# Kernel optimization log

Hardware: AMD Instinct MI355X
Metric: run time of the kernel (lower is better)

The kernel has to match this reference:

```python
import jax, jax.numpy as jnp
import numpy as np

LMAX = 5
L = LMAX + 1            # L_out = L_in = 6
DIM = L * L             # 36 spherical-harmonic coefficients
RES_B = 2 * L           # 12 beta points (Gauss-Legendre in cos(beta))
RES_A = 2 * L           # 12 alpha points (uniform)
CORRELATION = 3
REPEATS = np.arange(1, 2 * L, 2)  # [1,3,5,7,9,11]: ir.dim per l, mul=1 in irreps_out


def _normalized_assoc_legendre(lmax, x):
    """Fully (L2 on sphere) normalized associated Legendre Pbar_l^m(x), no CS phase.
    Returns dict[(l,m)] -> np.ndarray over x."""
    P = {}
    s = np.sqrt(np.maximum(1.0 - x * x, 0.0))
    P[(0, 0)] = np.full_like(x, np.sqrt(1.0 / (4.0 * np.pi)))
    for m in range(1, lmax + 1):
        P[(m, m)] = np.sqrt((2.0 * m + 1.0) / (2.0 * m)) * s * P[(m - 1, m - 1)]
    for m in range(0, lmax):
        P[(m + 1, m)] = np.sqrt(2.0 * m + 3.0) * x * P[(m, m)]
    for m in range(0, lmax + 1):
        for l in range(m + 2, lmax + 1):
            a = np.sqrt((4.0 * l * l - 1.0) / (l * l - m * m))
            b = np.sqrt(((l - 1.0) ** 2 - m * m) / (4.0 * (l - 1.0) ** 2 - 1.0))
            P[(l, m)] = a * (x * P[(l - 1, m)] - b * P[(l - 2, m)])
    return P


def build_s2grid(lmax, res_beta, res_alpha):
    """Y: [res_beta, res_alpha, (lmax+1)^2] real orthonormal SH samples.
    Yw: Y with quadrature weights so that einsum(f, Yw) inverts einsum(c, Y)."""
    xq, wq = np.polynomial.legendre.leggauss(res_beta)  # nodes in cos(beta)
    alpha = np.arange(res_alpha) * (2.0 * np.pi / res_alpha)
    P = _normalized_assoc_legendre(lmax, xq)
    dim = (lmax + 1) ** 2
    Y = np.zeros((res_beta, res_alpha, dim))
    sqrt2 = np.sqrt(2.0)
    for l in range(lmax + 1):
        for m in range(-l, l + 1):
            idx = l * l + l + m
            plm = P[(l, abs(m))]
            if m > 0:
                ang = sqrt2 * np.cos(m * alpha)
            elif m == 0:
                ang = np.ones(res_alpha)
            else:
                ang = sqrt2 * np.sin(-m * alpha)
            Y[:, :, idx] = plm[:, None] * ang[None, :]
    Yw = Y * wq[:, None, None] * (2.0 * np.pi / res_alpha)
    return jnp.asarray(Y, jnp.float32), jnp.asarray(Yw, jnp.float32)


def setup_inputs() -> dict:
    key = jax.random.key(0)
    k1, k2, k3 = jax.random.split(key, 3)
    atom_feat = jax.random.normal(k1, (4096, 128, DIM), dtype=jnp.float32)
    atom_type = jax.random.uniform(k2, (4096, 10), dtype=jnp.float32)
    weights = jax.random.normal(k3, (CORRELATION, 10, 128, L), dtype=jnp.float32)
    return {"atom_feat": atom_feat, "atom_type": atom_type, "weights": weights}


def reference(atom_feat, atom_type, weights):
    Y, Yw = build_s2grid(LMAX, RES_B, RES_A)

    def to_grid(c):      # [n, C, DIM] -> [n, C, beta, alpha]
        return jnp.einsum('nck,bak->ncba', c, Y)

    def from_grid(f):    # [n, C, beta, alpha] -> [n, C, DIM]
        return jnp.einsum('ncba,bak->nck', f, Yw)

    def apply_w(w):      # w: [E, C, L]; atom-type-weighted, expanded to DIM
        wn = jnp.einsum('ne,ecl->ncl', atom_type, w)  # [n, C, L]
        return jnp.repeat(wn, REPEATS, axis=-1, total_repeat_length=DIM)

    feat_grid = to_grid(atom_feat)  # reused across correlation orders
    prod = atom_feat
    result = apply_w(weights[0]) * prod
    for nu in range(1, CORRELATION):
        # Gaunt tensor product via S2 grid: pointwise multiply on the sphere
        prod = from_grid(to_grid(prod) * feat_grid)
        result = result + apply_w(weights[nu]) * prod
    return jnp.squeeze(result)
```

## Files before the change

### kernel.cpp

```cpp
#include <hip/hip_runtime.h>
#include <stdint.h>

namespace ct {

constexpr double PI_ = 3.14159265358979323846;

constexpr double csqrt(double x) {
  double g = x > 1.0 ? x : 1.0;
  for (int i = 0; i < 40; ++i) g = 0.5 * (g + x / g);
  return g;
}
constexpr double ccos(double x) {
  double x2 = x * x, t = 1.0, s = 1.0;
  for (int k = 1; k <= 16; ++k) { t *= -x2 / ((2.0 * k - 1.0) * (2.0 * k)); s += t; }
  return s;
}
constexpr double csin(double x) {
  double x2 = x * x, t = x, s = x;
  for (int k = 1; k <= 16; ++k) { t *= -x2 / ((2.0 * k) * (2.0 * k + 1.0)); s += t; }
  return s;
}

struct GL { double x[12]; double w[12]; };

constexpr GL gl12() {
  GL g{};
  for (int i = 0; i < 12; ++i) {
    double x = ccos(PI_ * (i + 0.75) / 12.5);
    for (int it = 0; it < 50; ++it) {
      double p0 = 1.0, p1 = x;
      for (int k = 2; k <= 12; ++k) { double pk = ((2.0 * k - 1.0) * x * p1 - (k - 1.0) * p0) / k; p0 = p1; p1 = pk; }
      double dp = 12.0 * (x * p1 - p0) / (x * x - 1.0);
      x -= p1 / dp;
    }
    double p0 = 1.0, p1 = x;
    for (int k = 2; k <= 12; ++k) { double pk = ((2.0 * k - 1.0) * x * p1 - (k - 1.0) * p0) / k; p0 = p1; p1 = pk; }
    double dp = 12.0 * (x * p1 - p0) / (x * x - 1.0);
    g.x[i] = x;
    g.w[i] = 2.0 / ((1.0 - x * x) * dp * dp);
  }
  return g;
}

struct Tab {
  double PA[12][36];
  double PB[12][36];
  double ANG[12][36];
};

constexpr Tab make_tab() {
  Tab t{};
  GL g = gl12();
  for (int b = 0; b < 12; ++b) {
    double x = g.x[b];
    double s = csqrt(1.0 - x * x);
    double P[6][6] = {};
    P[0][0] = csqrt(1.0 / (4.0 * PI_));
    for (int m = 1; m <= 5; ++m) P[m][m] = csqrt((2.0 * m + 1.0) / (2.0 * m)) * s * P[m - 1][m - 1];
    for (int m = 0; m < 5; ++m)  P[m + 1][m] = csqrt(2.0 * m + 3.0) * x * P[m][m];
    for (int m = 0; m <= 5; ++m)
      for (int l = m + 2; l <= 5; ++l) {
        double aa = csqrt((4.0 * l * l - 1.0) / (double)(l * l - m * m));
        double bb = csqrt(((l - 1.0) * (l - 1.0) - (double)(m * m)) / (4.0 * (l - 1.0) * (l - 1.0) - 1.0));
        P[l][m] = aa * (x * P[l - 1][m] - bb * P[l - 2][m]);
      }
    for (int l = 0; l <= 5; ++l)
      for (int m = -l; m <= l; ++m) {
        int k = l * l + l + m, am = m < 0 ? -m : m;
        t.PA[b][k] = P[l][am];
        t.PB[b][k] = P[l][am] * g.w[b] * (2.0 * PI_ / 12.0);
      }
  }
  double r2 = csqrt(2.0);
  for (int a = 0; a < 12; ++a)
    for (int l = 0; l <= 5; ++l)
      for (int m = -l; m <= l; ++m) {
        int k = l * l + l + m, am = m < 0 ? -m : m;
        double v = 1.0;
        if (m != 0) {
          int qq = (am * a) % 12;
          double ang = 2.0 * PI_ * qq / 12.0;
          if (ang > PI_) ang -= 2.0 * PI_;
          v = (m > 0) ? r2 * ccos(ang) : r2 * csin(ang);
        }
        t.ANG[a][k] = v;
      }
  return t;
}

constexpr Tab TD = make_tab();

constexpr unsigned f2bf(double x) {
  if (x == 0.0) return 0u;
  unsigned s = 0u; double a = x;
  if (a < 0.0) { s = 0x8000u; a = -a; }
  int e = 127;
  while (a >= 2.0) { a *= 0.5; ++e; }
  while (a < 1.0)  { a *= 2.0; --e; }
  double md = (a - 1.0) * 128.0;
  int mi = (int)md;
  double fr = md - mi;
  if (fr > 0.5 || (fr == 0.5 && (mi & 1))) ++mi;
  if (mi == 128) { mi = 0; ++e; }
  return s | ((unsigned)e << 7) | (unsigned)mi;
}

constexpr double syn_val(int k, int n) {
  if (k >= 36 || n >= 144) return 0.0;
  int b = n / 12, a = n % 12;
  return TD.PA[b][k] * TD.ANG[a][k];
}
constexpr double ana_val(int kp, int np) {
  if (kp >= 144 || np >= 36) return 0.0;
  int b = kp / 12, a = kp % 12;
  return TD.PB[b][np] * TD.ANG[a][np];
}

struct alignas(16) Syn32 { unsigned v[3 * 5 * 64 * 4]; };
struct alignas(16) Ana32 { unsigned v[9 * 2 * 64 * 4]; };

constexpr Syn32 make_syn32() {
  Syn32 F{};
  for (int ks = 0; ks < 3; ++ks)
    for (int nt = 0; nt < 5; ++nt)
      for (int lane = 0; lane < 64; ++lane)
        for (int jp = 0; jp < 4; ++jp) {
          int h = lane >> 5, n = nt * 32 + (lane & 31);
          int k0 = ks * 16 + h * 8 + jp * 2;
          F.v[((ks * 5 + nt) * 64 + lane) * 4 + jp] =
              f2bf(syn_val(k0, n)) | (f2bf(syn_val(k0 + 1, n)) << 16);
        }
  return F;
}
constexpr Ana32 make_ana32() {
  Ana32 F{};
  for (int ks = 0; ks < 9; ++ks)
    for (int nt = 0; nt < 2; ++nt)
      for (int lane = 0; lane < 64; ++lane)
        for (int jp = 0; jp < 4; ++jp) {
          int h = lane >> 5, n = nt * 32 + (lane & 31);
          int k0 = ks * 16 + h * 8 + jp * 2;
          F.v[((ks * 2 + nt) * 64 + lane) * 4 + jp] =
              f2bf(ana_val(k0, n)) | (f2bf(ana_val(k0 + 1, n)) << 16);
        }
  return F;
}

}

__device__ constexpr ct::Syn32 SYNB = ct::make_syn32();
__device__ constexpr ct::Ana32 ANAB = ct::make_ana32();

typedef __attribute__((ext_vector_type(8))) short short8;
typedef __attribute__((ext_vector_type(16))) float f32x16;

union S8 { short8 s; unsigned u[4]; uint2 u2[2]; };

__device__ __forceinline__ unsigned short bfr(float x) {
  return (unsigned short)((__float_as_uint(x) + 0x8000u) >> 16);
}
__device__ __forceinline__ unsigned pk2(float x, float y) {
  return (unsigned)bfr(x) | ((unsigned)bfr(y) << 16);
}

__device__ __forceinline__ short8 fr16(const uint4* p) {
  uint4 t = *p; S8 r; r.u[0] = t.x; r.u[1] = t.y; r.u[2] = t.z; r.u[3] = t.w;
  return r.s;
}

__device__ __forceinline__ S8 mkfrag(unsigned P0, unsigned P1, unsigned Q0, unsigned Q1) {
  auto r0 = __builtin_amdgcn_permlane32_swap((int)P0, (int)Q0, false, false);
  auto r1 = __builtin_amdgcn_permlane32_swap((int)P1, (int)Q1, false, false);
  S8 f;
  f.u[0] = (unsigned)r0[0];
  f.u[1] = (unsigned)r1[0];
  f.u[2] = (unsigned)r0[1];
  f.u[3] = (unsigned)r1[1];
  return f;
}

#define Z16 {0.f,0.f,0.f,0.f,0.f,0.f,0.f,0.f,0.f,0.f,0.f,0.f,0.f,0.f,0.f,0.f}

__global__ __launch_bounds__(256, 1)
void gaunt32_kernel(const float* __restrict__ feat,
                    const float* __restrict__ atype,
                    const float* __restrict__ wts,
                    float* __restrict__ out) {
  __shared__ uint4 TAB[2112];

  const int tid = threadIdx.x;
  const int lane = tid & 63;
  const int m = lane & 31, h = lane >> 5;
  const int mtile = blockIdx.x * 4 + (tid >> 6);
  const int rowbase = mtile * 32;
  const int atom = mtile >> 2;
  const int chb = (mtile & 3) * 32;

  {
    const uint4* s4 = reinterpret_cast<const uint4*>(SYNB.v);
    const uint4* a4 = reinterpret_cast<const uint4*>(ANAB.v);
#pragma unroll
    for (int i = 0; i < 4; ++i) {
      int idx = tid + 256 * i;
      if (idx < 960) TAB[idx] = s4[idx];
    }
#pragma unroll
    for (int i = 0; i < 5; ++i) {
      int idx = tid + 256 * i;
      if (idx < 1152) TAB[960 + idx] = a4[idx];
    }
  }

  const uint4* syn = TAB;
  const uint4* ana = TAB + 960;

  const float* fr = feat + (size_t)(rowbase + m) * 36;
  S8 af[3];
  {
    float4 a = *reinterpret_cast<const float4*>(fr + h * 8);
    float4 b = *reinterpret_cast<const float4*>(fr + h * 8 + 4);
    af[0].u[0] = pk2(a.x, a.y); af[0].u[1] = pk2(a.z, a.w);
    af[0].u[2] = pk2(b.x, b.y); af[0].u[3] = pk2(b.z, b.w);
    a = *reinterpret_cast<const float4*>(fr + 16 + h * 8);
    b = *reinterpret_cast<const float4*>(fr + 20 + h * 8);
    af[1].u[0] = pk2(a.x, a.y); af[1].u[1] = pk2(a.z, a.w);
    af[1].u[2] = pk2(b.x, b.y); af[1].u[3] = pk2(b.z, b.w);
    af[2].u[0] = 0; af[2].u[1] = 0; af[2].u[2] = 0; af[2].u[3] = 0;
    if (h == 0) {
      a = *reinterpret_cast<const float4*>(fr + 32);
      af[2].u[0] = pk2(a.x, a.y); af[2].u[1] = pk2(a.z, a.w);
    }
  }

  float wnv[3][6];
  {
    const float* ab = atype + atom * 10;
    float at_[10];
#pragma unroll
    for (int e = 0; e < 10; ++e) at_[e] = ab[e];
    const float* wb = wts + (size_t)(chb + m) * 6;
#pragma unroll
    for (int nu = 0; nu < 3; ++nu) {
#pragma unroll
      for (int l = 0; l < 6; ++l) wnv[nu][l] = 0.f;
#pragma unroll
      for (int e = 0; e < 10; ++e) {
        const float* p = wb + (size_t)(nu * 10 + e) * 768;
        float2 x = *reinterpret_cast<const float2*>(p);
        float2 y = *reinterpret_cast<const float2*>(p + 2);
        float2 z = *reinterpret_cast<const float2*>(p + 4);
        wnv[nu][0] += at_[e] * x.x; wnv[nu][1] += at_[e] * x.y;
        wnv[nu][2] += at_[e] * y.x; wnv[nu][3] += at_[e] * y.y;
        wnv[nu][4] += at_[e] * z.x; wnv[nu][5] += at_[e] * z.y;
      }
    }
  }

  constexpr int LC0t[4][4] = {{0,1,1,1},{2,3,3,3},{4,4,4,4},{4,5,5,5}};
  constexpr int LC1t[4][4] = {{2,2,2,2},{3,3,3,3},{4,4,4,4},{5,5,5,5}};

  float ovg[4][4];
  float ov5[4];
  {
#pragma unroll
    for (int g = 0; g < 4; ++g) {
      float4 c = *reinterpret_cast<const float4*>(fr + 8 * g + 4 * h);
      const float* cp = reinterpret_cast<const float*>(&c);
#pragma unroll
      for (int i = 0; i < 4; ++i) {
        const float w0 = h ? wnv[0][LC1t[g][i]] : wnv[0][LC0t[g][i]];
        ovg[g][i] = w0 * cp[i];
      }
    }
    float4 c5 = {0.f, 0.f, 0.f, 0.f};
    if (h == 0) c5 = *reinterpret_cast<const float4*>(fr + 32);
    const float* cp = reinterpret_cast<const float*>(&c5);
#pragma unroll
    for (int i = 0; i < 4; ++i) ov5[i] = wnv[0][5] * cp[i];
  }

  __syncthreads();

  f32x16 p1[2]; p1[0] = (f32x16)Z16; p1[1] = (f32x16)Z16;
#pragma unroll
  for (int mt = 0; mt < 5; ++mt) {
    f32x16 a1 = Z16;
#pragma unroll
    for (int ks = 0; ks < 3; ++ks)
      a1 = __builtin_amdgcn_mfma_f32_32x32x16_bf16(fr16(syn + (ks * 5 + mt) * 64 + lane),
                                                   af[ks].s, a1, 0, 0, 0);
#pragma unroll
    for (int q = 0; q < 2; ++q) {
      const int ksg = 2 * mt + q;
      if (ksg < 9) {
        S8 fb = mkfrag(pk2(a1[8*q+0]*a1[8*q+0], a1[8*q+1]*a1[8*q+1]),
                       pk2(a1[8*q+2]*a1[8*q+2], a1[8*q+3]*a1[8*q+3]),
                       pk2(a1[8*q+4]*a1[8*q+4], a1[8*q+5]*a1[8*q+5]),
                       pk2(a1[8*q+6]*a1[8*q+6], a1[8*q+7]*a1[8*q+7]));
        p1[0] = __builtin_amdgcn_mfma_f32_32x32x16_bf16(fr16(ana + (ksg * 2 + 0) * 64 + lane),
                                                        fb.s, p1[0], 0, 0, 0);
        p1[1] = __builtin_amdgcn_mfma_f32_32x32x16_bf16(fr16(ana + (ksg * 2 + 1) * 64 + lane),
                                                        fb.s, p1[1], 0, 0, 0);
      }
    }
  }

#pragma unroll
  for (int g = 0; g < 4; ++g)
#pragma unroll
    for (int i = 0; i < 4; ++i) {
      const float w1 = h ? wnv[1][LC1t[g][i]] : wnv[1][LC0t[g][i]];
      ovg[g][i] += w1 * p1[0][4 * g + i];
    }
#pragma unroll
  for (int i = 0; i < 4; ++i) ov5[i] += wnv[1][5] * p1[1][i];

  S8 b3[3];
  b3[0] = mkfrag(pk2(p1[0][0],  p1[0][1]),  pk2(p1[0][2],  p1[0][3]),
                 pk2(p1[0][4],  p1[0][5]),  pk2(p1[0][6],  p1[0][7]));
  b3[1] = mkfrag(pk2(p1[0][8],  p1[0][9]),  pk2(p1[0][10], p1[0][11]),
                 pk2(p1[0][12], p1[0][13]), pk2(p1[0][14], p1[0][15]));
  b3[2] = mkfrag(pk2(p1[1][0],  p1[1][1]),  pk2(p1[1][2],  p1[1][3]),
                 pk2(p1[1][4],  p1[1][5]),  pk2(p1[1][6],  p1[1][7]));

  f32x16 p2[2]; p2[0] = (f32x16)Z16; p2[1] = (f32x16)Z16;
#pragma unroll
  for (int mt = 0; mt < 5; ++mt) {
    f32x16 a1 = Z16, a3 = Z16;
#pragma unroll
    for (int ks = 0; ks < 3; ++ks) {
      short8 y = fr16(syn + (ks * 5 + mt) * 64 + lane);
      a1 = __builtin_amdgcn_mfma_f32_32x32x16_bf16(y, af[ks].s, a1, 0, 0, 0);
      a3 = __builtin_amdgcn_mfma_f32_32x32x16_bf16(y, b3[ks].s, a3, 0, 0, 0);
    }
#pragma unroll
    for (int q = 0; q < 2; ++q) {
      const int ksg = 2 * mt + q;
      if (ksg < 9) {
        S8 gb = mkfrag(pk2(a3[8*q+0]*a1[8*q+0], a3[8*q+1]*a1[8*q+1]),
                       pk2(a3[8*q+2]*a1[8*q+2], a3[8*q+3]*a1[8*q+3]),
                       pk2(a3[8*q+4]*a1[8*q+4], a3[8*q+5]*a1[8*q+5]),
                       pk2(a3[8*q+6]*a1[8*q+6], a3[8*q+7]*a1[8*q+7]));
        p2[0] = __builtin_amdgcn_mfma_f32_32x32x16_bf16(fr16(ana + (ksg * 2 + 0) * 64 + lane),
                                                        gb.s, p2[0], 0, 0, 0);
        p2[1] = __builtin_amdgcn_mfma_f32_32x32x16_bf16(fr16(ana + (ksg * 2 + 1) * 64 + lane),
                                                        gb.s, p2[1], 0, 0, 0);
      }
    }
  }

  float* o0 = out + (size_t)(rowbase + m) * 36;
#pragma unroll
  for (int g = 0; g < 4; ++g) {
    float ov[4];
#pragma unroll
    for (int i = 0; i < 4; ++i) {
      const float w2 = h ? wnv[2][LC1t[g][i]] : wnv[2][LC0t[g][i]];
      ov[i] = ovg[g][i] + w2 * p2[0][4 * g + i];
    }
    float4 o4 = {ov[0], ov[1], ov[2], ov[3]};
    *reinterpret_cast<float4*>(o0 + 8 * g + 4 * h) = o4;
  }
  if (h == 0) {
    float ov[4];
#pragma unroll
    for (int i = 0; i < 4; ++i) ov[i] = ov5[i] + wnv[2][5] * p2[1][i];
    float4 o4 = {ov[0], ov[1], ov[2], ov[3]};
    *reinterpret_cast<float4*>(o0 + 32) = o4;
  }
}

extern "C" void kernel_launch(void* const* d_in, const int* in_sizes, int n_in,
                              void* d_out, int out_size, void* d_ws, size_t ws_size,
                              hipStream_t stream) {
  const float* feat = (const float*)d_in[0];
  const float* atype = (const float*)d_in[1];
  const float* wts = (const float*)d_in[2];
  float* out = (float*)d_out;
  (void)in_sizes; (void)n_in; (void)out_size; (void)d_ws; (void)ws_size;

  gaunt32_kernel<<<4096, 256, 0, stream>>>(feat, atype, wts, out);
}
```

Measured before the change: 235.7 us.

## Make kernel persistent over 8 tiles per wave with next-tile feature prefetch

Cuts the grid from 4096 to 512 blocks. Each wave now loops over 8 row tiles with a stride of 2048, so the shared-memory table load and barrier are paid once per block instead of once per tile. Inside the loop, the next tile's features and atom types are loaded into registers while the current tile's MFMA work runs, to hide global latency. The trade-off is higher register pressure, and with launch_bounds(256,1) and only 512 blocks there may be too few waves per CU to hide latency.

```diff
diff --git a/kernel.cpp b/kernel.cpp
--- a/kernel.cpp
+++ b/kernel.cpp
@@ -180,6 +180,7 @@
 }
 
 #define Z16 {0.f,0.f,0.f,0.f,0.f,0.f,0.f,0.f,0.f,0.f,0.f,0.f,0.f,0.f,0.f,0.f}
+#define F4Z {0.f,0.f,0.f,0.f}
 
 __global__ __launch_bounds__(256, 1)
 void gaunt32_kernel(const float* __restrict__ feat,
@@ -191,10 +192,8 @@
   const int tid = threadIdx.x;
   const int lane = tid & 63;
   const int m = lane & 31, h = lane >> 5;
-  const int mtile = blockIdx.x * 4 + (tid >> 6);
-  const int rowbase = mtile * 32;
-  const int atom = mtile >> 2;
-  const int chb = (mtile & 3) * 32;
+  const int wgid = blockIdx.x * 4 + (tid >> 6);
+  const int chb = (wgid & 3) * 32;
 
   {
     const uint4* s4 = reinterpret_cast<const uint4*>(SYNB.v);
@@ -214,31 +213,63 @@
   const uint4* syn = TAB;
   const uint4* ana = TAB + 960;
 
-  const float* fr = feat + (size_t)(rowbase + m) * 36;
-  S8 af[3];
+  constexpr int LC0t[4][4] = {{0,1,1,1},{2,3,3,3},{4,4,4,4},{4,5,5,5}};
+  constexpr int LC1t[4][4] = {{2,2,2,2},{3,3,3,3},{4,4,4,4},{5,5,5,5}};
+
+  const float* wb = wts + (size_t)(chb + m) * 6;
+
+  float4 r0, r1, r2, r3, r4;
+  float at_[10];
   {
-    float4 a = *reinterpret_cast<const float4*>(fr + h * 8);
-    float4 b = *reinterpret_cast<const float4*>(fr + h * 8 + 4);
-    af[0].u[0] = pk2(a.x, a.y); af[0].u[1] = pk2(a.z, a.w);
-    af[0].u[2] = pk2(b.x, b.y); af[0].u[3] = pk2(b.z, b.w);
-    a = *reinterpret_cast<const float4*>(fr + 16 + h * 8);
-    b = *reinterpret_cast<const float4*>(fr + 20 + h * 8);
-    af[1].u[0] = pk2(a.x, a.y); af[1].u[1] = pk2(a.z, a.w);
-    af[1].u[2] = pk2(b.x, b.y); af[1].u[3] = pk2(b.z, b.w);
+    const float* fp = feat + (size_t)(wgid * 32 + m) * 36;
+    r0 = *reinterpret_cast<const float4*>(fp + h * 8);
+    r1 = *reinterpret_cast<const float4*>(fp + h * 8 + 4);
+    r2 = *reinterpret_cast<const float4*>(fp + 16 + h * 8);
+    r3 = *reinterpret_cast<const float4*>(fp + 20 + h * 8);
+    r4 = (float4)F4Z;
+    if (h == 0) r4 = *reinterpret_cast<const float4*>(fp + 32);
+    const float* ab = atype + (size_t)(wgid >> 2) * 10;
+#pragma unroll
+    for (int e = 0; e < 10; ++e) at_[e] = ab[e];
+  }
+
+  __syncthreads();
+
+#pragma unroll 1
+  for (int t = 0; t < 8; ++t) {
+    const int mtile = wgid + t * 2048;
+    const int rowbase = mtile * 32;
+    const float* fr = feat + (size_t)(rowbase + m) * 36;
+
+    S8 af[3];
+    af[0].u[0] = pk2(r0.x, r0.y); af[0].u[1] = pk2(r0.z, r0.w);
+    af[0].u[2] = pk2(r1.x, r1.y); af[0].u[3] = pk2(r1.z, r1.w);
+    af[1].u[0] = pk2(r2.x, r2.y); af[1].u[1] = pk2(r2.z, r2.w);
+    af[1].u[2] = pk2(r3.x, r3.y); af[1].u[3] = pk2(r3.z, r3.w);
     af[2].u[0] = 0; af[2].u[1] = 0; af[2].u[2] = 0; af[2].u[3] = 0;
     if (h == 0) {
-      a = *reinterpret_cast<const float4*>(fr + 32);
-      af[2].u[0] = pk2(a.x, a.y); af[2].u[1] = pk2(a.z, a.w);
-    }
-  }
-
-  float wnv[3][6];
-  {
-    const float* ab = atype + atom * 10;
-    float at_[10];
-#pragma unroll
-    for (int e = 0; e < 10; ++e) at_[e] = ab[e];
-    const float* wb = wts + (size_t)(chb + m) * 6;
+      af[2].u[0] = pk2(r4.x, r4.y); af[2].u[1] = pk2(r4.z, r4.w);
+    }
+
+    float4 n0 = (float4)F4Z, n1 = (float4)F4Z, n2 = (float4)F4Z,
+           n3 = (float4)F4Z, n4 = (float4)F4Z;
+    float nat[10];
+#pragma unroll
+    for (int e = 0; e < 10; ++e) nat[e] = 0.f;
+    if (t < 7) {
+      const int mtn = wgid + (t + 1) * 2048;
+      const float* fp = feat + (size_t)(mtn * 32 + m) * 36;
+      n0 = *reinterpret_cast<const float4*>(fp + h * 8);
+      n1 = *reinterpret_cast<const float4*>(fp + h * 8 + 4);
+      n2 = *reinterpret_cast<const float4*>(fp + 16 + h * 8);
+      n3 = *reinterpret_cast<const float4*>(fp + 20 + h * 8);
+      if (h == 0) n4 = *reinterpret_cast<const float4*>(fp + 32);
+      const float* ab = atype + (size_t)(mtn >> 2) * 10;
+#pragma unroll
+      for (int e = 0; e < 10; ++e) nat[e] = ab[e];
+    }
+
+    float wnv[3][6];
 #pragma unroll
     for (int nu = 0; nu < 3; ++nu) {
 #pragma unroll
@@ -254,119 +285,118 @@
         wnv[nu][4] += at_[e] * z.x; wnv[nu][5] += at_[e] * z.y;
       }
     }
-  }
-
-  constexpr int LC0t[4][4] = {{0,1,1,1},{2,3,3,3},{4,4,4,4},{4,5,5,5}};
-  constexpr int LC1t[4][4] = {{2,2,2,2},{3,3,3,3},{4,4,4,4},{5,5,5,5}};
-
-  float ovg[4][4];
-  float ov5[4];
-  {
+
+    float ovg[4][4];
+    float ov5[4];
+    {
+#pragma unroll
+      for (int g = 0; g < 4; ++g) {
+        float4 c = *reinterpret_cast<const float4*>(fr + 8 * g + 4 * h);
+        const float* cp = reinterpret_cast<const float*>(&c);
+#pragma unroll
+        for (int i = 0; i < 4; ++i) {
+          const float w0 = h ? wnv[0][LC1t[g][i]] : wnv[0][LC0t[g][i]];
+          ovg[g][i] = w0 * cp[i];
+        }
+      }
+      float4 c5 = (float4)F4Z;
+      if (h == 0) c5 = *reinterpret_cast<const float4*>(fr + 32);
+      const float* cp = reinterpret_cast<const float*>(&c5);
+#pragma unroll
+      for (int i = 0; i < 4; ++i) ov5[i] = wnv[0][5] * cp[i];
+    }
+
+    f32x16 p1[2]; p1[0] = (f32x16)Z16; p1[1] = (f32x16)Z16;
+#pragma unroll
+    for (int mt = 0; mt < 5; ++mt) {
+      f32x16 a1 = Z16;
+#pragma unroll
+      for (int ks = 0; ks < 3; ++ks)
+        a1 = __builtin_amdgcn_mfma_f32_32x32x16_bf16(fr16(syn + (ks * 5 + mt) * 64 + lane),
+                                                     af[ks].s, a1, 0, 0, 0);
+#pragma unroll
+      for (int q = 0; q < 2; ++q) {
+        const int ksg = 2 * mt + q;
+        if (ksg < 9) {
+          S8 fb = mkfrag(pk2(a1[8*q+0]*a1[8*q+0], a1[8*q+1]*a1[8*q+1]),
+                         pk2(a1[8*q+2]*a1[8*q+2], a1[8*q+3]*a1[8*q+3]),
+                         pk2(a1[8*q+4]*a1[8*q+4], a1[8*q+5]*a1[8*q+5]),
+                         pk2(a1[8*q+6]*a1[8*q+6], a1[8*q+7]*a1[8*q+7]));
+          p1[0] = __builtin_amdgcn_mfma_f32_32x32x16_bf16(fr16(ana + (ksg * 2 + 0) * 64 + lane),
+                                                          fb.s, p1[0], 0, 0, 0);
+          p1[1] = __builtin_amdgcn_mfma_f32_32x32x16_bf16(fr16(ana + (ksg * 2 + 1) * 64 + lane),
+                                                          fb.s, p1[1], 0, 0, 0);
+        }
+      }
+    }
+
+#pragma unroll
+    for (int g = 0; g < 4; ++g)
+#pragma unroll
+      for (int i = 0; i < 4; ++i) {
+        const float w1 = h ? wnv[1][LC1t[g][i]] : wnv[1][LC0t[g][i]];
+        ovg[g][i] += w1 * p1[0][4 * g + i];
+      }
+#pragma unroll
+    for (int i = 0; i < 4; ++i) ov5[i] += wnv[1][5] * p1[1][i];
+
+    S8 b3[3];
+    b3[0] = mkfrag(pk2(p1[0][0],  p1[0][1]),  pk2(p1[0][2],  p1[0][3]),
+                   pk2(p1[0][4],  p1[0][5]),  pk2(p1[0][6],  p1[0][7]));
+    b3[1] = mkfrag(pk2(p1[0][8],  p1[0][9]),  pk2(p1[0][10], p1[0][11]),
+                   pk2(p1[0][12], p1[0][13]), pk2(p1[0][14], p1[0][15]));
+    b3[2] = mkfrag(pk2(p1[1][0],  p1[1][1]),  pk2(p1[1][2],  p1[1][3]),
+                   pk2(p1[1][4],  p1[1][5]),  pk2(p1[1][6],  p1[1][7]));
+
+    f32x16 p2[2]; p2[0] = (f32x16)Z16; p2[1] = (f32x16)Z16;
+#pragma unroll
+    for (int mt = 0; mt < 5; ++mt) {
+      f32x16 a1 = Z16, a3 = Z16;
+#pragma unroll
+      for (int ks = 0; ks < 3; ++ks) {
+        short8 y = fr16(syn + (ks * 5 + mt) * 64 + lane);
+        a1 = __builtin_amdgcn_mfma_f32_32x32x16_bf16(y, af[ks].s, a1, 0, 0, 0);
+        a3 = __builtin_amdgcn_mfma_f32_32x32x16_bf16(y, b3[ks].s, a3, 0, 0, 0);
+      }
+#pragma unroll
+      for (int q = 0; q < 2; ++q) {
+        const int ksg = 2 * mt + q;
+        if (ksg < 9) {
+          S8 gb = mkfrag(pk2(a3[8*q+0]*a1[8*q+0], a3[8*q+1]*a1[8*q+1]),
+                         pk2(a3[8*q+2]*a1[8*q+2], a3[8*q+3]*a1[8*q+3]),
+                         pk2(a3[8*q+4]*a1[8*q+4], a3[8*q+5]*a1[8*q+5]),
+                         pk2(a3[8*q+6]*a1[8*q+6], a3[8*q+7]*a1[8*q+7]));
+          p2[0] = __builtin_amdgcn_mfma_f32_32x32x16_bf16(fr16(ana + (ksg * 2 + 0) * 64 + lane),
+                                                          gb.s, p2[0], 0, 0, 0);
+          p2[1] = __builtin_amdgcn_mfma_f32_32x32x16_bf16(fr16(ana + (ksg * 2 + 1) * 64 + lane),
+                                                          gb.s, p2[1], 0, 0, 0);
+        }
+      }
+    }
+
+    float* o0 = out + (size_t)(rowbase + m) * 36;
 #pragma unroll
     for (int g = 0; g < 4; ++g) {
-      float4 c = *reinterpret_cast<const float4*>(fr + 8 * g + 4 * h);
-      const float* cp = reinterpret_cast<const float*>(&c);
+      float ov[4];
 #pragma unroll
       for (int i = 0; i < 4; ++i) {
-        const float w0 = h ? wnv[0][LC1t[g][i]] : wnv[0][LC0t[g][i]];
-        ovg[g][i] = w0 * cp[i];
-      }
-    }
-    float4 c5 = {0.f, 0.f, 0.f, 0.f};
-    if (h == 0) c5 = *reinterpret_cast<const float4*>(fr + 32);
-    const float* cp = reinterpret_cast<const float*>(&c5);
-#pragma unroll
-    for (int i = 0; i < 4; ++i) ov5[i] = wnv[0][5] * cp[i];
-  }
-
-  __syncthreads();
-
-  f32x16 p1[2]; p1[0] = (f32x16)Z16; p1[1] = (f32x16)Z16;
-#pragma unroll
-  for (int mt = 0; mt < 5; ++mt) {
-    f32x16 a1 = Z16;
-#pragma unroll
-    for (int ks = 0; ks < 3; ++ks)
-      a1 = __builtin_amdgcn_mfma_f32_32x32x16_bf16(fr16(syn + (ks * 5 + mt) * 64 + lane),
-                                                   af[ks].s, a1, 0, 0, 0);
-#pragma unroll
-    for (int q = 0; q < 2; ++q) {
-      const int ksg = 2 * mt + q;
-      if (ksg < 9) {
-        S8 fb = mkfrag(pk2(a1[8*q+0]*a1[8*q+0], a1[8*q+1]*a1[8*q+1]),
-                       pk2(a1[8*q+2]*a1[8*q+2], a1[8*q+3]*a1[8*q+3]),
-                       pk2(a1[8*q+4]*a1[8*q+4], a1[8*q+5]*a1[8*q+5]),
-                       pk2(a1[8*q+6]*a1[8*q+6], a1[8*q+7]*a1[8*q+7]));
-        p1[0] = __builtin_amdgcn_mfma_f32_32x32x16_bf16(fr16(ana + (ksg * 2 + 0) * 64 + lane),
-                                                        fb.s, p1[0], 0, 0, 0);
-        p1[1] = __builtin_amdgcn_mfma_f32_32x32x16_bf16(fr16(ana + (ksg * 2 + 1) * 64 + lane),
-                                                        fb.s, p1[1], 0, 0, 0);
-      }
-    }
-  }
-
-#pragma unroll
-  for (int g = 0; g < 4; ++g)
-#pragma unroll
-    for (int i = 0; i < 4; ++i) {
-      const float w1 = h ? wnv[1][LC1t[g][i]] : wnv[1][LC0t[g][i]];
-      ovg[g][i] += w1 * p1[0][4 * g + i];
-    }
-#pragma unroll
-  for (int i = 0; i < 4; ++i) ov5[i] += wnv[1][5] * p1[1][i];
-
-  S8 b3[3];
-  b3[0] = mkfrag(pk2(p1[0][0],  p1[0][1]),  pk2(p1[0][2],  p1[0][3]),
-                 pk2(p1[0][4],  p1[0][5]),  pk2(p1[0][6],  p1[0][7]));
-  b3[1] = mkfrag(pk2(p1[0][8],  p1[0][9]),  pk2(p1[0][10], p1[0][11]),
-                 pk2(p1[0][12], p1[0][13]), pk2(p1[0][14], p1[0][15]));
-  b3[2] = mkfrag(pk2(p1[1][0],  p1[1][1]),  pk2(p1[1][2],  p1[1][3]),
-                 pk2(p1[1][4],  p1[1][5]),  pk2(p1[1][6],  p1[1][7]));
-
-  f32x16 p2[2]; p2[0] = (f32x16)Z16; p2[1] = (f32x16)Z16;
-#pragma unroll
-  for (int mt = 0; mt < 5; ++mt) {
-    f32x16 a1 = Z16, a3 = Z16;
-#pragma unroll
-    for (int ks = 0; ks < 3; ++ks) {
-      short8 y = fr16(syn + (ks * 5 + mt) * 64 + lane);
-      a1 = __builtin_amdgcn_mfma_f32_32x32x16_bf16(y, af[ks].s, a1, 0, 0, 0);
-      a3 = __builtin_amdgcn_mfma_f32_32x32x16_bf16(y, b3[ks].s, a3, 0, 0, 0);
-    }
-#pragma unroll
-    for (int q = 0; q < 2; ++q) {
-      const int ksg = 2 * mt + q;
-      if (ksg < 9) {
-        S8 gb = mkfrag(pk2(a3[8*q+0]*a1[8*q+0], a3[8*q+1]*a1[8*q+1]),
-                       pk2(a3[8*q+2]*a1[8*q+2], a3[8*q+3]*a1[8*q+3]),
-                       pk2(a3[8*q+4]*a1[8*q+4], a3[8*q+5]*a1[8*q+5]),
-                       pk2(a3[8*q+6]*a1[8*q+6], a3[8*q+7]*a1[8*q+7]));
-        p2[0] = __builtin_amdgcn_mfma_f32_32x32x16_bf16(fr16(ana + (ksg * 2 + 0) * 64 + lane),
-                                                        gb.s, p2[0], 0, 0, 0);
-        p2[1] = __builtin_amdgcn_mfma_f32_32x32x16_bf16(fr16(ana + (ksg * 2 + 1) * 64 + lane),
-                                                        gb.s, p2[1], 0, 0, 0);
-      }
-    }
-  }
-
-  float* o0 = out + (size_t)(rowbase + m) * 36;
-#pragma unroll
-  for (int g = 0; g < 4; ++g) {
-    float ov[4];
-#pragma unroll
-    for (int i = 0; i < 4; ++i) {
-      const float w2 = h ? wnv[2][LC1t[g][i]] : wnv[2][LC0t[g][i]];
-      ov[i] = ovg[g][i] + w2 * p2[0][4 * g + i];
-    }
-    float4 o4 = {ov[0], ov[1], ov[2], ov[3]};
-    *reinterpret_cast<float4*>(o0 + 8 * g + 4 * h) = o4;
-  }
-  if (h == 0) {
-    float ov[4];
-#pragma unroll
-    for (int i = 0; i < 4; ++i) ov[i] = ov5[i] + wnv[2][5] * p2[1][i];
-    float4 o4 = {ov[0], ov[1], ov[2], ov[3]};
-    *reinterpret_cast<float4*>(o0 + 32) = o4;
+        const float w2 = h ? wnv[2][LC1t[g][i]] : wnv[2][LC0t[g][i]];
+        ov[i] = ovg[g][i] + w2 * p2[0][4 * g + i];
+      }
+      float4 o4 = {ov[0], ov[1], ov[2], ov[3]};
+      *reinterpret_cast<float4*>(o0 + 8 * g + 4 * h) = o4;
+    }
+    if (h == 0) {
+      float ov[4];
+#pragma unroll
+      for (int i = 0; i < 4; ++i) ov[i] = ov5[i] + wnv[2][5] * p2[1][i];
+      float4 o4 = {ov[0], ov[1], ov[2], ov[3]};
+      *reinterpret_cast<float4*>(o0 + 32) = o4;
+    }
+
+    r0 = n0; r1 = n1; r2 = n2; r3 = n3; r4 = n4;
+#pragma unroll
+    for (int e = 0; e < 10; ++e) at_[e] = nat[e];
   }
 }
 
@@ -379,5 +409,5 @@
   float* out = (float*)d_out;
   (void)in_sizes; (void)n_in; (void)out_size; (void)d_ws; (void)ws_size;
 
-  gaunt32_kernel<<<4096, 256, 0, stream>>>(feat, atype, wts, out);
-}
+  gaunt32_kernel<<<512, 256, 0, stream>>>(feat, atype, wts, out);
+}
```

Result: slower. 480.8 us (+104.0%).
